# Optimization experiments

Hardware: AMD Instinct MI355X
Metric: run time of the kernel (lower is better)

Reference implementation:

```python
import jax, jax.numpy as jnp
import numpy as np

B, S, D = 2, 8192, 1024
H, HD, FD = 16, 64, 256

def setup_inputs() -> dict:
    key = jax.random.key(0)
    ks = jax.random.split(key, 6)
    sc = 1.0 / np.sqrt(D)
    return {
        "hidden_states": jax.random.normal(ks[0], (B, S, D), jnp.float32),
        "Wq": jax.random.normal(ks[1], (D, D), jnp.float32) * sc,
        "Wk": jax.random.normal(ks[2], (D, D), jnp.float32) * sc,
        "Wv": jax.random.normal(ks[3], (D, D), jnp.float32) * sc,
        "Wo": jax.random.normal(ks[4], (D, D), jnp.float32) * sc,
        "Wf": jax.random.normal(ks[5], (FD, HD), jnp.float32) * (1.0 / np.sqrt(HD)),
    }

def reference(hidden_states, Wq, Wk, Wv, Wo, Wf):
    b, s, _ = hidden_states.shape
    # projections (torch Linear: x @ W.T), split heads -> (b, s, h, hd)
    q = (hidden_states @ Wq.T).reshape(b, s, H, HD)
    k = (hidden_states @ Wk.T).reshape(b, s, H, HD)
    v = (hidden_states @ Wv.T).reshape(b, s, H, HD)
    # elu+1 feature map -> (b, s, h, f)
    qf = jax.nn.elu(q @ Wf.T) + 1.0
    kf = jax.nn.elu(k @ Wf.T) + 1.0
    # global kv summary: (b, h, f, d)
    kv = jnp.einsum('bshf,bshd->bhfd', kf, v)
    out = jnp.einsum('bshf,bhfd->bshd', qf, kv)
    k_sum = kf.sum(axis=1)                       # (b, h, f)
    norm = jnp.einsum('bshf,bhf->bsh', qf, k_sum)[..., None] + 1e-6
    out = (out / norm).reshape(b, s, D)
    return out @ Wo.T
```

## Files before the change

kernel.cpp:

```cpp
#include <hip/hip_runtime.h>
#include <stdint.h>

typedef __bf16 bf16_t;
typedef __attribute__((ext_vector_type(8))) __bf16 bfv8;
typedef __attribute__((ext_vector_type(4))) __bf16 bfv4;
typedef __attribute__((ext_vector_type(4))) float f32x4;

constexpr int BATCH = 2, SEQ = 8192, DIM = 1024, NH = 16, HDIM = 64, FDIM = 256;
constexpr int MROWS = BATCH * SEQ;
constexpr int NCHUNK = 16;
constexpr int KV_NIT = (SEQ / NCHUNK) / 32;
constexpr int KVP_CH = 32 * 256 * 68;

__device__ __forceinline__ f32x4 mfma_bf16(bfv8 a, bfv8 b, f32x4 c) {
  return __builtin_amdgcn_mfma_f32_16x16x32_bf16(a, b, c, 0, 0, 0);
}

__device__ __forceinline__ void gload_lds16(const bf16_t* g, bf16_t* lds) {
  auto const* gp = reinterpret_cast<const __attribute__((address_space(1))) uint32_t*>(
      reinterpret_cast<uintptr_t>(g));
  auto* lp = reinterpret_cast<__attribute__((address_space(3))) uint32_t*>(
      reinterpret_cast<uintptr_t>(lds));
  __builtin_amdgcn_global_load_lds(gp, lp, 16, 0, 0);
}

__device__ __forceinline__ void stage128x64(const bf16_t* g_base, int k0,
                                            bf16_t* lds, int wid, int lane) {
#pragma unroll
  for (int j = 0; j < 4; ++j) {
    int r0 = (wid * 4 + j) * 8;
    int g_row = r0 + (lane >> 3);
    int g_slot = (lane & 7) ^ (g_row & 7);
    const bf16_t* src = g_base + (size_t)g_row * DIM + k0 + g_slot * 8;
    gload_lds16(src, lds + r0 * 64);
  }
}

__global__ __launch_bounds__(256) void cvt_all(const float* __restrict__ X,
                                               const float* __restrict__ Wq,
                                               const float* __restrict__ Wk,
                                               const float* __restrict__ Wv,
                                               const float* __restrict__ Wo,
                                               const float* __restrict__ Wf,
                                               bf16_t* __restrict__ Xb,
                                               bf16_t* __restrict__ W3,
                                               bf16_t* __restrict__ Wob,
                                               bf16_t* __restrict__ Wfb) {
  int i = blockIdx.x * 256 + threadIdx.x;
  const float* src;
  bf16_t* dst;
  int off;
  if (i < 4194304) {
    src = X; dst = Xb; off = i;
  } else {
    int j = i - 4194304;
    if (j < 786432) {
      int seg = j >> 18;
      off = j & 262143;
      src = (seg == 0) ? Wq : ((seg == 1) ? Wk : Wv);
      dst = W3 + (size_t)seg * 1048576;
    } else if (j < 1048576) {
      off = j - 786432; src = Wo; dst = Wob;
    } else {
      off = j - 1048576; src = Wf; dst = Wfb;
    }
  }
  float4 v = reinterpret_cast<const float4*>(src)[off];
  bfv4 o = {(__bf16)v.x, (__bf16)v.y, (__bf16)v.z, (__bf16)v.w};
  reinterpret_cast<bfv4*>(dst)[off] = o;
}

__global__ __launch_bounds__(256) void gemm_qkv(const bf16_t* __restrict__ A,
                                                const bf16_t* __restrict__ Wall,
                                                bf16_t* __restrict__ Q,
                                                bf16_t* __restrict__ K,
                                                bf16_t* __restrict__ V) {
  __shared__ bf16_t As[2][128 * 64];
  __shared__ bf16_t Bs[2][128 * 64];
  int z = blockIdx.z;
  const bf16_t* Wm = Wall + (size_t)z * (DIM * DIM);
  bf16_t* C = (z == 0) ? Q : ((z == 1) ? K : V);
  int lane = threadIdx.x & 63, wid = threadIdx.x >> 6;
  int lr = lane & 15, lg = lane >> 4;
  int wr = wid >> 1, wc = wid & 1;
  int brow = blockIdx.x * 128, bcol = blockIdx.y * 128;
  const bf16_t* Ab = A + (size_t)brow * DIM;
  const bf16_t* Bb = Wm + (size_t)bcol * DIM;
  f32x4 acc[4][4] = {};

  stage128x64(Ab, 0, As[0], wid, lane);
  stage128x64(Bb, 0, Bs[0], wid, lane);
  asm volatile("s_waitcnt vmcnt(0)" ::: "memory");
  __builtin_amdgcn_s_barrier();

  auto TILE = [&](const bf16_t* Acur, const bf16_t* Bcur, bf16_t* Anext, bf16_t* Bnext,
                  int knext) __attribute__((always_inline)) {
    if (knext < DIM) {
      stage128x64(Ab, knext, Anext, wid, lane);
      stage128x64(Bb, knext, Bnext, wid, lane);
    }
#pragma unroll
    for (int kk = 0; kk < 2; ++kk) {
      bfv8 af[4], bg[4];
#pragma unroll
      for (int t = 0; t < 4; ++t) {
        int ar = wr * 64 + t * 16 + lr;
        af[t] = *reinterpret_cast<const bfv8*>(&Acur[ar * 64 + (((kk * 4 + lg) ^ (ar & 7)) * 8)]);
        int br = wc * 64 + t * 16 + lr;
        bg[t] = *reinterpret_cast<const bfv8*>(&Bcur[br * 64 + (((kk * 4 + lg) ^ (br & 7)) * 8)]);
      }
#pragma unroll
      for (int i = 0; i < 4; ++i)
#pragma unroll
        for (int j = 0; j < 4; ++j) acc[i][j] = mfma_bf16(af[i], bg[j], acc[i][j]);
    }
    asm volatile("s_waitcnt vmcnt(0)" ::: "memory");
    __builtin_amdgcn_s_barrier();
  };

  for (int ks = 0; ks < DIM / 64; ks += 2) {
    TILE(As[0], Bs[0], As[1], Bs[1], (ks + 1) * 64);
    TILE(As[1], Bs[1], As[0], Bs[0], (ks + 2) * 64);
  }

#pragma unroll
  for (int i = 0; i < 4; ++i) {
    int r = brow + wr * 64 + i * 16 + lg * 4;
#pragma unroll
    for (int j = 0; j < 4; ++j) {
      int c = bcol + wc * 64 + j * 16 + lr;
#pragma unroll
      for (int q = 0; q < 4; ++q) C[(size_t)(r + q) * DIM + c] = (__bf16)acc[i][j][q];
    }
  }
}

__global__ __launch_bounds__(256) void gemm_final(const bf16_t* __restrict__ A,
                                                  const bf16_t* __restrict__ W,
                                                  float* __restrict__ C) {
  __shared__ bf16_t As[2][128 * 64];
  __shared__ bf16_t Bs[2][128 * 64];
  int lane = threadIdx.x & 63, wid = threadIdx.x >> 6;
  int lr = lane & 15, lg = lane >> 4;
  int wr = wid >> 1, wc = wid & 1;
  int brow = blockIdx.x * 128, bcol = blockIdx.y * 128;
  const bf16_t* Ab = A + (size_t)brow * DIM;
  const bf16_t* Bb = W + (size_t)bcol * DIM;
  f32x4 acc[4][4] = {};

  stage128x64(Ab, 0, As[0], wid, lane);
  stage128x64(Bb, 0, Bs[0], wid, lane);
  asm volatile("s_waitcnt vmcnt(0)" ::: "memory");
  __builtin_amdgcn_s_barrier();

  auto TILE = [&](const bf16_t* Acur, const bf16_t* Bcur, bf16_t* Anext, bf16_t* Bnext,
                  int knext) __attribute__((always_inline)) {
    if (knext < DIM) {
      stage128x64(Ab, knext, Anext, wid, lane);
      stage128x64(Bb, knext, Bnext, wid, lane);
    }
#pragma unroll
    for (int kk = 0; kk < 2; ++kk) {
      bfv8 af[4], bg[4];
#pragma unroll
      for (int t = 0; t < 4; ++t) {
        int ar = wr * 64 + t * 16 + lr;
        af[t] = *reinterpret_cast<const bfv8*>(&Acur[ar * 64 + (((kk * 4 + lg) ^ (ar & 7)) * 8)]);
        int br = wc * 64 + t * 16 + lr;
        bg[t] = *reinterpret_cast<const bfv8*>(&Bcur[br * 64 + (((kk * 4 + lg) ^ (br & 7)) * 8)]);
      }
#pragma unroll
      for (int i = 0; i < 4; ++i)
#pragma unroll
        for (int j = 0; j < 4; ++j) acc[i][j] = mfma_bf16(af[i], bg[j], acc[i][j]);
    }
    asm volatile("s_waitcnt vmcnt(0)" ::: "memory");
    __builtin_amdgcn_s_barrier();
  };

  for (int ks = 0; ks < DIM / 64; ks += 2) {
    TILE(As[0], Bs[0], As[1], Bs[1], (ks + 1) * 64);
    TILE(As[1], Bs[1], As[0], Bs[0], (ks + 2) * 64);
  }

#pragma unroll
  for (int i = 0; i < 4; ++i) {
    int r = brow + wr * 64 + i * 16 + lg * 4;
#pragma unroll
    for (int j = 0; j < 4; ++j) {
      int c = bcol + wc * 64 + j * 16 + lr;
#pragma unroll
      for (int q = 0; q < 4; ++q) C[(size_t)(r + q) * DIM + c] = acc[i][j][q];
    }
  }
}

__global__ __launch_bounds__(256, 2) void kv_fused(const bf16_t* __restrict__ Kb,
                                                   const bf16_t* __restrict__ Vb,
                                                   const bf16_t* __restrict__ Wf,
                                                   float* __restrict__ kv_part) {
  __shared__ bf16_t kf_lds[4][64 * 36];
  __shared__ bf16_t vt[4][80 * 36];
  int chunk = blockIdx.x, bh = blockIdx.y;
  int b = bh >> 4, h = bh & 15;
  int lane = threadIdx.x & 63, wid = threadIdx.x >> 6;
  int lr = lane & 15, lg = lane >> 4;
  int f0 = wid * 64;
  for (int i = lane; i < 16 * 36; i += 64) {
    int n = i / 36, s = i - n * 36;
    vt[wid][(64 + n) * 36 + s] = (n == 0) ? (__bf16)1.0f : (__bf16)0.0f;
  }
  bfv8 wf[4][2];
#pragma unroll
  for (int ft = 0; ft < 4; ++ft)
#pragma unroll
    for (int kk = 0; kk < 2; ++kk)
      wf[ft][kk] = *reinterpret_cast<const bfv8*>(Wf + (size_t)(f0 + ft * 16 + lr) * HDIM + kk * 32 + lg * 8);
  const bf16_t* Kbase = Kb + (size_t)b * SEQ * DIM + h * HDIM;
  const bf16_t* Vbase = Vb + (size_t)b * SEQ * DIM + h * HDIM;
  int s0 = chunk * (SEQ / NCHUNK);

  bfv8 krgA[2][2], krgB[2][2];
#pragma unroll
  for (int st = 0; st < 2; ++st)
#pragma unroll
    for (int kk = 0; kk < 2; ++kk)
      krgA[st][kk] = *reinterpret_cast<const bfv8*>(Kbase + (size_t)(s0 + st * 16 + lr) * DIM + kk * 32 + lg * 8);

  f32x4 acc[4][5] = {};

  auto STEP = [&](int it, bfv8(&krgC)[2][2], bfv8(&krgN)[2][2]) __attribute__((always_inline)) {
    int sb = s0 + it * 32;
    bfv8 vv[4];
#pragma unroll
    for (int rep = 0; rep < 4; ++rep) {
      int idx = rep * 64 + lane;
      vv[rep] = *reinterpret_cast<const bfv8*>(Vbase + (size_t)(sb + (idx >> 3)) * DIM + (idx & 7) * 8);
    }
    if (it + 1 < KV_NIT) {
#pragma unroll
      for (int st = 0; st < 2; ++st)
#pragma unroll
        for (int kk = 0; kk < 2; ++kk)
          krgN[st][kk] = *reinterpret_cast<const bfv8*>(Kbase + (size_t)(sb + 32 + st * 16 + lr) * DIM + kk * 32 + lg * 8);
    }
    f32x4 ckf[4][2] = {};
#pragma unroll
    for (int ft = 0; ft < 4; ++ft)
#pragma unroll
      for (int st = 0; st < 2; ++st)
#pragma unroll
        for (int kk = 0; kk < 2; ++kk) ckf[ft][st] = mfma_bf16(wf[ft][kk], krgC[st][kk], ckf[ft][st]);
#pragma unroll
    for (int rep = 0; rep < 4; ++rep) {
      int idx = rep * 64 + lane;
#pragma unroll
      for (int j = 0; j < 8; ++j) vt[wid][((idx & 7) * 8 + j) * 36 + (idx >> 3)] = vv[rep][j];
    }
#pragma unroll
    for (int ft = 0; ft < 4; ++ft)
#pragma unroll
      for (int st = 0; st < 2; ++st)
#pragma unroll
        for (int q = 0; q < 4; ++q) {
          float x = ckf[ft][st][q];
          x = (x > 0.0f) ? (x + 1.0f) : __expf(x);
          kf_lds[wid][(ft * 16 + lg * 4 + q) * 36 + st * 16 + lr] = (__bf16)x;
        }
    bfv8 af[4], bg[5];
#pragma unroll
    for (int ft = 0; ft < 4; ++ft)
      af[ft] = *reinterpret_cast<const bfv8*>(&kf_lds[wid][(ft * 16 + lr) * 36 + lg * 8]);
#pragma unroll
    for (int nt = 0; nt < 5; ++nt)
      bg[nt] = *reinterpret_cast<const bfv8*>(&vt[wid][(nt * 16 + lr) * 36 + lg * 8]);
#pragma unroll
    for (int ft = 0; ft < 4; ++ft)
#pragma unroll
      for (int nt = 0; nt < 5; ++nt) acc[ft][nt] = mfma_bf16(af[ft], bg[nt], acc[ft][nt]);
  };

  for (int it2 = 0; it2 < KV_NIT; it2 += 2) {
    STEP(it2, krgA, krgB);
    STEP(it2 + 1, krgB, krgA);
  }

  float* outb = kv_part + ((size_t)chunk * 32 + bh) * (FDIM * 68);
#pragma unroll
  for (int ft = 0; ft < 4; ++ft)
#pragma unroll
    for (int q = 0; q < 4; ++q) {
      int f = f0 + ft * 16 + lg * 4 + q;
#pragma unroll
      for (int nt = 0; nt < 4; ++nt)
        outb[(size_t)f * 68 + nt * 16 + lr] = acc[ft][nt][q];
      if (lr < 4) outb[(size_t)f * 68 + 64 + lr] = acc[ft][4][q];
    }
}

__global__ __launch_bounds__(256) void kv_reduce(const float* __restrict__ part,
                                                 bf16_t* __restrict__ kvT) {
  int i = blockIdx.x * 256 + threadIdx.x;
  if (i < KVP_CH) {
    int n = i % 68;
    int t = i / 68;
    int f = t & 255, bh = t >> 8;
    float s = 0.0f;
#pragma unroll
    for (int c = 0; c < NCHUNK; ++c) s += part[(size_t)c * KVP_CH + i];
    int fs = ((((f >> 3) ^ (n & 7)) << 3) | (f & 7));
    kvT[((size_t)bh * 80 + n) * FDIM + fs] = (__bf16)s;
  } else {
    int j = i - KVP_CH;
    int f = j & 255;
    int t = j >> 8;
    int n = 68 + t % 12, bh = t / 12;
    kvT[((size_t)bh * 80 + n) * FDIM + f] = (__bf16)0.0f;
  }
}

__global__ __launch_bounds__(256) void attn_fused(const bf16_t* __restrict__ Qb,
                                                  const bf16_t* __restrict__ Wf,
                                                  const bf16_t* __restrict__ kvT,
                                                  bf16_t* __restrict__ outp) {
  __shared__ bf16_t qf_lds[64 * 264];
  __shared__ bf16_t kv_lds[80 * 256];
  int rb = blockIdx.x, h = blockIdx.y;
  int row0 = rb * 64;
  int bh = (row0 >> 13) * NH + h;
  int lane = threadIdx.x & 63, wid = threadIdx.x >> 6;
  int lr = lane & 15, lg = lane >> 4;
  int f0 = wid * 64;
  const bf16_t* kvTb = kvT + (size_t)bh * 80 * FDIM;
#pragma unroll
  for (int i = 0; i < 10; ++i) {
    int sbase = wid * 640 + i * 64;
    gload_lds16(kvTb + (size_t)(sbase + lane) * 8, kv_lds + sbase * 8);
  }
  bfv8 qa[4][2], wfb[4][2];
#pragma unroll
  for (int t = 0; t < 4; ++t)
#pragma unroll
    for (int kk = 0; kk < 2; ++kk) {
      qa[t][kk] = *reinterpret_cast<const bfv8*>(Qb + (size_t)(row0 + t * 16 + lr) * DIM + h * HDIM + kk * 32 + lg * 8);
      wfb[t][kk] = *reinterpret_cast<const bfv8*>(Wf + (size_t)(f0 + t * 16 + lr) * HDIM + kk * 32 + lg * 8);
    }
  f32x4 cq[4][4] = {};
#pragma unroll
  for (int rt = 0; rt < 4; ++rt)
#pragma unroll
    for (int ft = 0; ft < 4; ++ft)
#pragma unroll
      for (int kk = 0; kk < 2; ++kk) cq[rt][ft] = mfma_bf16(qa[rt][kk], wfb[ft][kk], cq[rt][ft]);
#pragma unroll
  for (int rt = 0; rt < 4; ++rt)
#pragma unroll
    for (int ft = 0; ft < 4; ++ft)
#pragma unroll
      for (int q = 0; q < 4; ++q) {
        float x = cq[rt][ft][q];
        x = (x > 0.0f) ? (x + 1.0f) : __expf(x);
        qf_lds[(size_t)(rt * 16 + lg * 4 + q) * 264 + f0 + ft * 16 + lr] = (__bf16)x;
      }
  __syncthreads();
  f32x4 acc[5] = {};
#pragma unroll
  for (int ks = 0; ks < 8; ++ks) {
    bfv8 a = *reinterpret_cast<const bfv8*>(&qf_lds[(size_t)(wid * 16 + lr) * 264 + ks * 32 + lg * 8]);
#pragma unroll
    for (int nt = 0; nt < 5; ++nt) {
      bfv8 bg = *reinterpret_cast<const bfv8*>(
          &kv_lds[(size_t)(nt * 16 + lr) * 256 + (((ks * 4 + lg) ^ (lr & 7)) * 8)]);
      acc[nt] = mfma_bf16(a, bg, acc[nt]);
    }
  }
  __syncthreads();
#pragma unroll
  for (int q = 0; q < 4; ++q) {
    float nrm = __shfl(acc[4][q], (lane & 48)) + 1e-6f;
    int row = wid * 16 + lg * 4 + q;
#pragma unroll
    for (int nt = 0; nt < 4; ++nt)
      qf_lds[(size_t)row * 264 + nt * 16 + lr] = (__bf16)(acc[nt][q] / nrm);
  }
  __syncthreads();
#pragma unroll
  for (int rep = 0; rep < 2; ++rep) {
    int id = rep * 256 + threadIdx.x;
    int row = id >> 3, c8 = id & 7;
    bfv8 v = *reinterpret_cast<const bfv8*>(&qf_lds[(size_t)row * 264 + c8 * 8]);
    *reinterpret_cast<bfv8*>(&outp[(size_t)(row0 + row) * DIM + h * HDIM + c8 * 8]) = v;
  }
}

extern "C" void kernel_launch(void* const* d_in, const int* in_sizes, int n_in,
                              void* d_out, int out_size, void* d_ws, size_t ws_size,
                              hipStream_t stream) {
  const float* X  = (const float*)d_in[0];
  const float* Wq = (const float*)d_in[1];
  const float* Wk = (const float*)d_in[2];
  const float* Wv = (const float*)d_in[3];
  const float* Wo = (const float*)d_in[4];
  const float* Wf = (const float*)d_in[5];
  float* out = (float*)d_out;
  char* ws = (char*)d_ws;
  const size_t MB = 1ull << 20;
  if (ws_size < 75 * MB) return;

  bf16_t* Xb  = (bf16_t*)(ws + 0 * MB);
  bf16_t* W3  = (bf16_t*)(ws + 32 * MB);
  bf16_t* Qb  = (bf16_t*)(ws + 38 * MB);
  bf16_t* Wob = (bf16_t*)(ws + 70 * MB);
  bf16_t* Wfb = (bf16_t*)(ws + 72 * MB);
  bf16_t* kvT = (bf16_t*)(ws + 73 * MB);
  float* kv_part = (float*)(ws + 0 * MB);
  bf16_t* outp = (bf16_t*)(ws + 0 * MB);
  bf16_t* Kb = (bf16_t*)d_out;
  bf16_t* Vb = Kb + (size_t)MROWS * DIM;

  cvt_all<<<20496, 256, 0, stream>>>(X, Wq, Wk, Wv, Wo, Wf, Xb, W3, Wob, Wfb);

  gemm_qkv<<<dim3(128, 8, 3), 256, 0, stream>>>(Xb, W3, Qb, Kb, Vb);
  kv_fused<<<dim3(NCHUNK, 32), 256, 0, stream>>>(Kb, Vb, Wfb, kv_part);
  kv_reduce<<<2560, 256, 0, stream>>>(kv_part, kvT);
  attn_fused<<<dim3(256, NH), 256, 0, stream>>>(Qb, Wfb, kvT, outp);
  gemm_final<<<dim3(128, 8), 256, 0, stream>>>(outp, Wob, out);
}
```

Before: 283.2 us.

## Store V transposed from QKV GEMM and keep kf in registers in kv_fused

Result: slower. 291.7 us (+3.0%).

```diff
diff --git a/kernel.cpp b/kernel.cpp
--- a/kernel.cpp
+++ b/kernel.cpp
@@ -74,12 +74,14 @@
                                                 const bf16_t* __restrict__ Wall,
                                                 bf16_t* __restrict__ Q,
                                                 bf16_t* __restrict__ K,
-                                                bf16_t* __restrict__ V) {
-  __shared__ bf16_t As[2][128 * 64];
-  __shared__ bf16_t Bs[2][128 * 64];
+                                                bf16_t* __restrict__ Vt) {
+  __shared__ bf16_t smem[32768];
+  bf16_t* As0 = smem;
+  bf16_t* As1 = smem + 8192;
+  bf16_t* Bs0 = smem + 16384;
+  bf16_t* Bs1 = smem + 24576;
   int z = blockIdx.z;
   const bf16_t* Wm = Wall + (size_t)z * (DIM * DIM);
-  bf16_t* C = (z == 0) ? Q : ((z == 1) ? K : V);
   int lane = threadIdx.x & 63, wid = threadIdx.x >> 6;
   int lr = lane & 15, lg = lane >> 4;
   int wr = wid >> 1, wc = wid & 1;
@@ -88,8 +90,8 @@
   const bf16_t* Bb = Wm + (size_t)bcol * DIM;
   f32x4 acc[4][4] = {};
 
-  stage128x64(Ab, 0, As[0], wid, lane);
-  stage128x64(Bb, 0, Bs[0], wid, lane);
+  stage128x64(Ab, 0, As0, wid, lane);
+  stage128x64(Bb, 0, Bs0, wid, lane);
   asm volatile("s_waitcnt vmcnt(0)" ::: "memory");
   __builtin_amdgcn_s_barrier();
 
@@ -119,18 +121,45 @@
   };
 
   for (int ks = 0; ks < DIM / 64; ks += 2) {
-    TILE(As[0], Bs[0], As[1], Bs[1], (ks + 1) * 64);
-    TILE(As[1], Bs[1], As[0], Bs[0], (ks + 2) * 64);
-  }
-
-#pragma unroll
-  for (int i = 0; i < 4; ++i) {
-    int r = brow + wr * 64 + i * 16 + lg * 4;
-#pragma unroll
-    for (int j = 0; j < 4; ++j) {
-      int c = bcol + wc * 64 + j * 16 + lr;
-#pragma unroll
-      for (int q = 0; q < 4; ++q) C[(size_t)(r + q) * DIM + c] = (__bf16)acc[i][j][q];
+    TILE(As0, Bs0, As1, Bs1, (ks + 1) * 64);
+    TILE(As1, Bs1, As0, Bs0, (ks + 2) * 64);
+  }
+
+  if (z != 2) {
+    bf16_t* C = (z == 0) ? Q : K;
+#pragma unroll
+    for (int i = 0; i < 4; ++i) {
+      int r = brow + wr * 64 + i * 16 + lg * 4;
+#pragma unroll
+      for (int j = 0; j < 4; ++j) {
+        int c = bcol + wc * 64 + j * 16 + lr;
+#pragma unroll
+        for (int q = 0; q < 4; ++q) C[(size_t)(r + q) * DIM + c] = (__bf16)acc[i][j][q];
+      }
+    }
+  } else {
+    bf16_t* ldst = smem;
+#pragma unroll
+    for (int i = 0; i < 4; ++i)
+#pragma unroll
+      for (int j = 0; j < 4; ++j) {
+        int cl = wc * 64 + j * 16 + lr;
+        int sl = wr * 64 + i * 16 + lg * 4;
+        bfv4 v = {(__bf16)acc[i][j][0], (__bf16)acc[i][j][1],
+                  (__bf16)acc[i][j][2], (__bf16)acc[i][j][3]};
+        *reinterpret_cast<bfv4*>(&ldst[cl * 136 + sl]) = v;
+      }
+    __syncthreads();
+    int bb = brow >> 13;
+    int sg0 = brow & 8191;
+    bf16_t* Vtg = Vt + ((size_t)bb * DIM + bcol) * SEQ + sg0;
+    int sl8 = (threadIdx.x & 15) * 8;
+    int c0 = threadIdx.x >> 4;
+#pragma unroll
+    for (int rep = 0; rep < 8; ++rep) {
+      int cl = c0 + rep * 16;
+      bfv8 v = *reinterpret_cast<const bfv8*>(&ldst[cl * 136 + sl8]);
+      *reinterpret_cast<bfv8*>(&Vtg[(size_t)cl * SEQ + sl8]) = v;
     }
   }
 }
@@ -196,20 +225,14 @@
 }
 
 __global__ __launch_bounds__(256, 2) void kv_fused(const bf16_t* __restrict__ Kb,
-                                                   const bf16_t* __restrict__ Vb,
+                                                   const bf16_t* __restrict__ Vt,
                                                    const bf16_t* __restrict__ Wf,
                                                    float* __restrict__ kv_part) {
-  __shared__ bf16_t kf_lds[4][64 * 36];
-  __shared__ bf16_t vt[4][80 * 36];
   int chunk = blockIdx.x, bh = blockIdx.y;
   int b = bh >> 4, h = bh & 15;
   int lane = threadIdx.x & 63, wid = threadIdx.x >> 6;
   int lr = lane & 15, lg = lane >> 4;
   int f0 = wid * 64;
-  for (int i = lane; i < 16 * 36; i += 64) {
-    int n = i / 36, s = i - n * 36;
-    vt[wid][(64 + n) * 36 + s] = (n == 0) ? (__bf16)1.0f : (__bf16)0.0f;
-  }
   bfv8 wf[4][2];
 #pragma unroll
   for (int ft = 0; ft < 4; ++ft)
@@ -217,8 +240,11 @@
     for (int kk = 0; kk < 2; ++kk)
       wf[ft][kk] = *reinterpret_cast<const bfv8*>(Wf + (size_t)(f0 + ft * 16 + lr) * HDIM + kk * 32 + lg * 8);
   const bf16_t* Kbase = Kb + (size_t)b * SEQ * DIM + h * HDIM;
-  const bf16_t* Vbase = Vb + (size_t)b * SEQ * DIM + h * HDIM;
+  const bf16_t* Vtb = Vt + ((size_t)b * DIM + h * HDIM) * SEQ;
   int s0 = chunk * (SEQ / NCHUNK);
+  bfv8 ones;
+#pragma unroll
+  for (int j = 0; j < 8; ++j) ones[j] = (lr == 0) ? (__bf16)1.0f : (__bf16)0.0f;
 
   bfv8 krgA[2][2], krgB[2][2];
 #pragma unroll
@@ -231,11 +257,12 @@
 
   auto STEP = [&](int it, bfv8(&krgC)[2][2], bfv8(&krgN)[2][2]) __attribute__((always_inline)) {
     int sb = s0 + it * 32;
-    bfv8 vv[4];
-#pragma unroll
-    for (int rep = 0; rep < 4; ++rep) {
-      int idx = rep * 64 + lane;
-      vv[rep] = *reinterpret_cast<const bfv8*>(Vbase + (size_t)(sb + (idx >> 3)) * DIM + (idx & 7) * 8);
+    bfv4 bglo[4], bghi[4];
+#pragma unroll
+    for (int nt = 0; nt < 4; ++nt) {
+      const bf16_t* row = Vtb + (size_t)(nt * 16 + lr) * SEQ + sb;
+      bglo[nt] = *reinterpret_cast<const bfv4*>(row + lg * 4);
+      bghi[nt] = *reinterpret_cast<const bfv4*>(row + 16 + lg * 4);
     }
     if (it + 1 < KV_NIT) {
 #pragma unroll
@@ -244,40 +271,35 @@
         for (int kk = 0; kk < 2; ++kk)
           krgN[st][kk] = *reinterpret_cast<const bfv8*>(Kbase + (size_t)(sb + 32 + st * 16 + lr) * DIM + kk * 32 + lg * 8);
     }
-    f32x4 ckf[4][2] = {};
+    f32x4 ckf[2][4] = {};
+#pragma unroll
+    for (int st = 0; st < 2; ++st)
+#pragma unroll
+      for (int ft = 0; ft < 4; ++ft)
+#pragma unroll
+        for (int kk = 0; kk < 2; ++kk) ckf[st][ft] = mfma_bf16(krgC[st][kk], wf[ft][kk], ckf[st][ft]);
+    bfv8 af[4];
 #pragma unroll
     for (int ft = 0; ft < 4; ++ft)
 #pragma unroll
       for (int st = 0; st < 2; ++st)
 #pragma unroll
-        for (int kk = 0; kk < 2; ++kk) ckf[ft][st] = mfma_bf16(wf[ft][kk], krgC[st][kk], ckf[ft][st]);
-#pragma unroll
-    for (int rep = 0; rep < 4; ++rep) {
-      int idx = rep * 64 + lane;
-#pragma unroll
-      for (int j = 0; j < 8; ++j) vt[wid][((idx & 7) * 8 + j) * 36 + (idx >> 3)] = vv[rep][j];
-    }
-#pragma unroll
-    for (int ft = 0; ft < 4; ++ft)
-#pragma unroll
-      for (int st = 0; st < 2; ++st)
-#pragma unroll
         for (int q = 0; q < 4; ++q) {
-          float x = ckf[ft][st][q];
+          float x = ckf[st][ft][q];
           x = (x > 0.0f) ? (x + 1.0f) : __expf(x);
-          kf_lds[wid][(ft * 16 + lg * 4 + q) * 36 + st * 16 + lr] = (__bf16)x;
+          af[ft][st * 4 + q] = (__bf16)x;
         }
-    bfv8 af[4], bg[5];
-#pragma unroll
-    for (int ft = 0; ft < 4; ++ft)
-      af[ft] = *reinterpret_cast<const bfv8*>(&kf_lds[wid][(ft * 16 + lr) * 36 + lg * 8]);
-#pragma unroll
-    for (int nt = 0; nt < 5; ++nt)
-      bg[nt] = *reinterpret_cast<const bfv8*>(&vt[wid][(nt * 16 + lr) * 36 + lg * 8]);
-#pragma unroll
-    for (int ft = 0; ft < 4; ++ft)
-#pragma unroll
-      for (int nt = 0; nt < 5; ++nt) acc[ft][nt] = mfma_bf16(af[ft], bg[nt], acc[ft][nt]);
+#pragma unroll
+    for (int ft = 0; ft < 4; ++ft) {
+#pragma unroll
+      for (int nt = 0; nt < 4; ++nt) {
+        bfv8 bg;
+#pragma unroll
+        for (int e = 0; e < 4; ++e) { bg[e] = bglo[nt][e]; bg[4 + e] = bghi[nt][e]; }
+        acc[ft][nt] = mfma_bf16(af[ft], bg, acc[ft][nt]);
+      }
+      acc[ft][4] = mfma_bf16(af[ft], ones, acc[ft][4]);
+    }
   };
 
   for (int it2 = 0; it2 < KV_NIT; it2 += 2) {
@@ -416,12 +438,12 @@
   float* kv_part = (float*)(ws + 0 * MB);
   bf16_t* outp = (bf16_t*)(ws + 0 * MB);
   bf16_t* Kb = (bf16_t*)d_out;
-  bf16_t* Vb = Kb + (size_t)MROWS * DIM;
+  bf16_t* Vtb = Kb + (size_t)MROWS * DIM;
 
   cvt_all<<<20496, 256, 0, stream>>>(X, Wq, Wk, Wv, Wo, Wf, Xb, W3, Wob, Wfb);
 
-  gemm_qkv<<<dim3(128, 8, 3), 256, 0, stream>>>(Xb, W3, Qb, Kb, Vb);
-  kv_fused<<<dim3(NCHUNK, 32), 256, 0, stream>>>(Kb, Vb, Wfb, kv_part);
+  gemm_qkv<<<dim3(128, 8, 3), 256, 0, stream>>>(Xb, W3, Qb, Kb, Vtb);
+  kv_fused<<<dim3(NCHUNK, 32), 256, 0, stream>>>(Kb, Vtb, Wfb, kv_part);
   kv_reduce<<<2560, 256, 0, stream>>>(kv_part, kvT);
   attn_fused<<<dim3(256, NH), 256, 0, stream>>>(Qb, Wfb, kvT, outp);
   gemm_final<<<dim3(128, 8), 256, 0, stream>>>(outp, Wob, out);
```
